# Performance work log

Hardware: AMD Instinct MI355X
Metric: run time of the kernel (lower is better)

The kernel has to match this reference:

```python
import jax, jax.numpy as jnp
import numpy as np

EMBED_DIM = 1024
NUM_HEADS = 16
HEAD_DIM = EMBED_DIM // NUM_HEADS
SCALE = HEAD_DIM ** -0.5


def setup_inputs() -> dict:
    key = jax.random.key(0)
    ks = jax.random.split(key, 9)
    B, N = 2, 2048
    s = EMBED_DIM ** -0.5  # ~ torch Linear init scale
    x = jax.random.normal(ks[0], (B, N, EMBED_DIM), dtype=jnp.float32)
    Wq = jax.random.uniform(ks[1], (EMBED_DIM, EMBED_DIM), jnp.float32, -s, s)
    bq = jax.random.uniform(ks[2], (EMBED_DIM,), jnp.float32, -s, s)
    Wk = jax.random.uniform(ks[3], (EMBED_DIM, EMBED_DIM), jnp.float32, -s, s)
    bk = jax.random.uniform(ks[4], (EMBED_DIM,), jnp.float32, -s, s)
    Wv = jax.random.uniform(ks[5], (EMBED_DIM, EMBED_DIM), jnp.float32, -s, s)
    bv = jax.random.uniform(ks[6], (EMBED_DIM,), jnp.float32, -s, s)
    Wo = jax.random.uniform(ks[7], (EMBED_DIM, EMBED_DIM), jnp.float32, -s, s)
    bo = jax.random.uniform(ks[8], (EMBED_DIM,), jnp.float32, -s, s)
    return {"x": x, "Wq": Wq, "bq": bq, "Wk": Wk, "bk": bk,
            "Wv": Wv, "bv": bv, "Wo": Wo, "bo": bo}


def reference(x, Wq, bq, Wk, bk, Wv, bv, Wo, bo):
    B, N, R = x.shape
    H, D = NUM_HEADS, HEAD_DIM
    # projections: Linear(x) = x @ W^T + b; reshape to (B, H, N, D)
    def proj(W, b):
        return (x @ W.T + b).reshape(B, N, H, D).transpose(0, 2, 1, 3)
    q = proj(Wq, bq)
    k = proj(Wk, bk)
    v = proj(Wv, bv)
    attn = jnp.einsum('bhnd,bhmd->bhnm', q, k) * SCALE  # (B,H,N,N)
    attn = jax.nn.softmax(attn, axis=-1)
    out = jnp.einsum('bhnm,bhmd->bhnd', attn, v)        # (B,H,N,D)
    out = out.transpose(0, 2, 1, 3).reshape(B, N, R)
    return out @ Wo.T + bo
```

## Files before the change

### kernel.cpp

```cpp
#include <hip/hip_runtime.h>
#include <stdint.h>

typedef __bf16 bf16;
typedef __bf16 bf16x4 __attribute__((ext_vector_type(4)));
typedef __bf16 bf16x8 __attribute__((ext_vector_type(8)));
typedef float f32x4 __attribute__((ext_vector_type(4)));

#define MFMA16(a, b, c) __builtin_amdgcn_mfma_f32_16x16x32_bf16((a), (b), (c), 0, 0, 0)

#define EMBED 1024
#define SEQ   2048
#define MROWS 4096
#define ATTN_QSCALE 0.1803368801111f

__device__ __forceinline__ void gl2lds16(const bf16* g, bf16* l) {
    __builtin_amdgcn_global_load_lds(
        (const __attribute__((address_space(1))) void*)g,
        (__attribute__((address_space(3))) void*)l,
        16, 0, 0);
}

__global__ __launch_bounds__(256) void cast_all_kernel(
    const float* __restrict__ x,  const float* __restrict__ Wq,
    const float* __restrict__ Wk, const float* __restrict__ Wv,
    const float* __restrict__ Wo, bf16* __restrict__ dst) {
    const int blk = blockIdx.x;
    const float* src;
    size_t so, dofs;
    if (blk < 2048) {
        src = x; so = (size_t)blk * 2048; dofs = so;
    } else {
        const int w = (blk - 2048) >> 9;
        so  = (size_t)((blk - 2048) & 511) * 2048;
        src = (w == 0) ? Wq : (w == 1) ? Wk : (w == 2) ? Wv : Wo;
        dofs = (size_t)(4 + w) * 1024 * 1024 + so;
    }
    const size_t i = (size_t)threadIdx.x * 8;
    float4 a = *(const float4*)(src + so + i);
    float4 b = *(const float4*)(src + so + i + 4);
    bf16x8 o;
    o[0] = (bf16)a.x; o[1] = (bf16)a.y; o[2] = (bf16)a.z; o[3] = (bf16)a.w;
    o[4] = (bf16)b.x; o[5] = (bf16)b.y; o[6] = (bf16)b.z; o[7] = (bf16)b.w;
    *(bf16x8*)(dst + dofs + i) = o;
}

template <bool SCALE>
__device__ __forceinline__ void gemm_tile(const bf16* __restrict__ A,
                                          const bf16* __restrict__ W,
                                          const float* __restrict__ bias,
                                          bf16* __restrict__ C,
                                          int m0, int n0, bf16* smem) {
    const int lane = threadIdx.x & 63;
    const int wv   = threadIdx.x >> 6;
    const int wm   = (wv >> 1) * 64;
    const int wn   = (wv & 1) * 64;
    const int fr   = lane & 15;
    const int quad = lane >> 4;
    const int srow = wv * 16 + (lane >> 2);
    const int swz  = ((lane & 3) ^ ((lane >> 2) & 3) ^ ((lane >> 4) & 3)) * 8;
    const int fcol = (quad ^ (fr & 3) ^ (fr >> 2)) * 8;

    f32x4 acc[4][4];
#pragma unroll
    for (int mt = 0; mt < 4; ++mt)
#pragma unroll
        for (int nt = 0; nt < 4; ++nt)
            acc[mt][nt] = (f32x4){0.f, 0.f, 0.f, 0.f};

    auto stage = [&](int kt, int bb) {
        bf16* As = smem + bb * 8192;
        bf16* Bs = As + 4096;
        const int k0 = kt * 32;
#pragma unroll
        for (int c = 0; c < 2; ++c) {
            gl2lds16(A + (size_t)(m0 + c * 64 + srow) * 1024 + k0 + swz,
                     &As[(c * 64 + wv * 16) * 32]);
            gl2lds16(W + (size_t)(n0 + c * 64 + srow) * 1024 + k0 + swz,
                     &Bs[(c * 64 + wv * 16) * 32]);
        }
    };

    stage(0, 0);
    stage(1, 1);
#pragma unroll
    for (int kt = 0; kt < 32; ++kt) {
        if (kt < 31) asm volatile("s_waitcnt vmcnt(4)" ::: "memory");
        else         asm volatile("s_waitcnt vmcnt(0)" ::: "memory");
        __builtin_amdgcn_s_barrier();
        if (kt < 30) stage(kt + 2, (kt + 2) % 3);
        const bf16* As = smem + (kt % 3) * 8192;
        const bf16* Bs = As + 4096;
        bf16x8 af[4], bfr[4];
#pragma unroll
        for (int t = 0; t < 4; ++t) {
            af[t]  = *(const bf16x8*)&As[(wm + t * 16 + fr) * 32 + fcol];
            bfr[t] = *(const bf16x8*)&Bs[(wn + t * 16 + fr) * 32 + fcol];
        }
        __builtin_amdgcn_s_setprio(1);
#pragma unroll
        for (int mt = 0; mt < 4; ++mt)
#pragma unroll
            for (int nt = 0; nt < 4; ++nt)
                acc[mt][nt] = MFMA16(af[mt], bfr[nt], acc[mt][nt]);
        __builtin_amdgcn_s_setprio(0);
    }

    float bv[4];
#pragma unroll
    for (int nt = 0; nt < 4; ++nt)
        bv[nt] = bias[n0 + wn + nt * 16 + fr];
    const int row4 = quad * 4;
#pragma unroll
    for (int mt = 0; mt < 4; ++mt)
#pragma unroll
        for (int nt = 0; nt < 4; ++nt)
#pragma unroll
            for (int r = 0; r < 4; ++r) {
                int m = m0 + wm + mt * 16 + row4 + r;
                int n = n0 + wn + nt * 16 + fr;
                float v = acc[mt][nt][r] + bv[nt];
                if (SCALE) v *= ATTN_QSCALE;
                C[(size_t)m * 1024 + n] = (bf16)v;
            }
}

__device__ __forceinline__ void v_tile(const bf16* __restrict__ x,
                                       const bf16* __restrict__ Wv,
                                       const float* __restrict__ bias,
                                       bf16* __restrict__ VT,
                                       int m0, int n0, bf16* smem) {
    const int lane = threadIdx.x & 63;
    const int wv   = threadIdx.x >> 6;
    const int wmW  = (wv >> 1) * 64;
    const int wnT  = (wv & 1) * 64;
    const int f    = lane & 15;
    const int quad = lane >> 4;
    const int srow = wv * 16 + (lane >> 2);
    const int swz  = ((lane & 3) ^ ((lane >> 2) & 3) ^ ((lane >> 4) & 3)) * 8;
    const int fcol = (quad ^ (f & 3) ^ (f >> 2)) * 8;

    f32x4 acc[4][4];
#pragma unroll
    for (int mt = 0; mt < 4; ++mt)
#pragma unroll
        for (int nt = 0; nt < 4; ++nt)
            acc[mt][nt] = (f32x4){0.f, 0.f, 0.f, 0.f};

    auto stage = [&](int kt, int bb) {
        bf16* As = smem + bb * 8192;
        bf16* Bs = As + 4096;
        const int k0 = kt * 32;
#pragma unroll
        for (int c = 0; c < 2; ++c) {
            gl2lds16(x  + (size_t)(m0 + c * 64 + srow) * 1024 + k0 + swz,
                     &As[(c * 64 + wv * 16) * 32]);
            gl2lds16(Wv + (size_t)(n0 + c * 64 + srow) * 1024 + k0 + swz,
                     &Bs[(c * 64 + wv * 16) * 32]);
        }
    };

    stage(0, 0);
    stage(1, 1);
#pragma unroll
    for (int kt = 0; kt < 32; ++kt) {
        if (kt < 31) asm volatile("s_waitcnt vmcnt(4)" ::: "memory");
        else         asm volatile("s_waitcnt vmcnt(0)" ::: "memory");
        __builtin_amdgcn_s_barrier();
        if (kt < 30) stage(kt + 2, (kt + 2) % 3);
        const bf16* As = smem + (kt % 3) * 8192;
        const bf16* Bs = As + 4096;
        bf16x8 wf[4], xf[4];
#pragma unroll
        for (int t = 0; t < 4; ++t) {
            wf[t] = *(const bf16x8*)&Bs[(wmW + t * 16 + f) * 32 + fcol];
            xf[t] = *(const bf16x8*)&As[(wnT + t * 16 + f) * 32 + fcol];
        }
        __builtin_amdgcn_s_setprio(1);
#pragma unroll
        for (int mt = 0; mt < 4; ++mt)
#pragma unroll
            for (int nt = 0; nt < 4; ++nt)
                acc[mt][nt] = MFMA16(wf[mt], xf[nt], acc[mt][nt]);
        __builtin_amdgcn_s_setprio(0);
    }

    float4 b4[4];
#pragma unroll
    for (int mt = 0; mt < 4; ++mt)
        b4[mt] = *(const float4*)&bias[n0 + wmW + mt * 16 + quad * 4];

    __syncthreads();

#pragma unroll
    for (int mt = 0; mt < 4; ++mt)
#pragma unroll
        for (int nt = 0; nt < 4; ++nt) {
            const int tok = wnT + nt * 16 + f;
#pragma unroll
            for (int r = 0; r < 4; ++r) {
                const float bvr = (r == 0) ? b4[mt].x : (r == 1) ? b4[mt].y
                                : (r == 2) ? b4[mt].z : b4[mt].w;
                smem[(wmW + mt * 16 + quad * 4 + r) * 136 + tok] =
                    (bf16)(acc[mt][nt][r] + bvr);
            }
        }
    __syncthreads();

    const int n_r  = threadIdx.x >> 4;
    const int t8   = (threadIdx.x & 15) * 8;
    const int base = t8 & ~31;
    const int u4   = ((t8 >> 3) & 3) * 4;
    const int bb   = m0 >> 11;
    const int tokg = (m0 & 2047) + t8;
#pragma unroll
    for (int p = 0; p < 8; ++p) {
        const int n_loc = p * 16 + n_r;
        const bf16* row = &smem[n_loc * 136];
        bf16x4 a = *(const bf16x4*)&row[base + u4];
        bf16x4 b = *(const bf16x4*)&row[base + 16 + u4];
        bf16x8 v = {a[0], a[1], a[2], a[3], b[0], b[1], b[2], b[3]};
        *(bf16x8*)&VT[((size_t)(bb * 1024 + n0 + n_loc)) * 2048 + tokg] = v;
    }
}

__global__ __launch_bounds__(256) void qkv_kernel(
    const bf16* __restrict__ x,
    const bf16* __restrict__ Wq, const float* __restrict__ bq,
    const bf16* __restrict__ Wk, const float* __restrict__ bk,
    const bf16* __restrict__ Wv, const float* __restrict__ bv,
    bf16* __restrict__ Q, bf16* __restrict__ K, bf16* __restrict__ VT) {
    __shared__ __align__(16) bf16 smem[24576];
    const int m0    = blockIdx.x * 128;
    const int which = blockIdx.y >> 3;
    const int n0    = (blockIdx.y & 7) * 128;
    if (which == 0)      gemm_tile<true>(x, Wq, bq, Q, m0, n0, smem);
    else if (which == 1) gemm_tile<false>(x, Wk, bk, K, m0, n0, smem);
    else                 v_tile(x, Wv, bv, VT, m0, n0, smem);
}

__global__ __launch_bounds__(256) void oproj_kernel(
    const bf16* __restrict__ A, const bf16* __restrict__ W,
    const float* __restrict__ bias, float* __restrict__ C) {
    const int m0 = blockIdx.x * 128;
    const int n0 = blockIdx.y * 64;

    __shared__ __align__(16) bf16 smem[18432];

    const int lane = threadIdx.x & 63;
    const int wv   = threadIdx.x >> 6;
    const int wm   = (wv >> 1) * 64;
    const int wn   = (wv & 1) * 32;
    const int fr   = lane & 15;
    const int quad = lane >> 4;
    const int srow = wv * 16 + (lane >> 2);
    const int swz  = ((lane & 3) ^ ((lane >> 2) & 3) ^ ((lane >> 4) & 3)) * 8;
    const int fcol = (quad ^ (fr & 3) ^ (fr >> 2)) * 8;

    f32x4 acc[4][2];
#pragma unroll
    for (int mt = 0; mt < 4; ++mt)
#pragma unroll
        for (int nt = 0; nt < 2; ++nt)
            acc[mt][nt] = (f32x4){0.f, 0.f, 0.f, 0.f};

    auto stage = [&](int kt, int bb) {
        bf16* As = smem + bb * 6144;
        bf16* Bs = As + 4096;
        const int k0 = kt * 32;
#pragma unroll
        for (int c = 0; c < 2; ++c)
            gl2lds16(A + (size_t)(m0 + c * 64 + srow) * 1024 + k0 + swz,
                     &As[(c * 64 + wv * 16) * 32]);
        gl2lds16(W + (size_t)(n0 + srow) * 1024 + k0 + swz,
                 &Bs[(wv * 16) * 32]);
    };

    stage(0, 0);
    stage(1, 1);
#pragma unroll
    for (int kt = 0; kt < 32; ++kt) {
        if (kt < 31) asm volatile("s_waitcnt vmcnt(3)" ::: "memory");
        else         asm volatile("s_waitcnt vmcnt(0)" ::: "memory");
        __builtin_amdgcn_s_barrier();
        if (kt < 30) stage(kt + 2, (kt + 2) % 3);
        const bf16* As = smem + (kt % 3) * 6144;
        const bf16* Bs = As + 4096;
        bf16x8 af[4], bfr[2];
#pragma unroll
        for (int t = 0; t < 4; ++t)
            af[t] = *(const bf16x8*)&As[(wm + t * 16 + fr) * 32 + fcol];
#pragma unroll
        for (int t = 0; t < 2; ++t)
            bfr[t] = *(const bf16x8*)&Bs[(wn + t * 16 + fr) * 32 + fcol];
        __builtin_amdgcn_s_setprio(1);
#pragma unroll
        for (int mt = 0; mt < 4; ++mt)
#pragma unroll
            for (int nt = 0; nt < 2; ++nt)
                acc[mt][nt] = MFMA16(af[mt], bfr[nt], acc[mt][nt]);
        __builtin_amdgcn_s_setprio(0);
    }

    float bv[2];
#pragma unroll
    for (int nt = 0; nt < 2; ++nt)
        bv[nt] = bias[n0 + wn + nt * 16 + fr];
    const int row4 = quad * 4;
#pragma unroll
    for (int mt = 0; mt < 4; ++mt)
#pragma unroll
        for (int nt = 0; nt < 2; ++nt)
#pragma unroll
            for (int r = 0; r < 4; ++r) {
                int m = m0 + wm + mt * 16 + row4 + r;
                int n = n0 + wn + nt * 16 + fr;
                C[(size_t)m * 1024 + n] = acc[mt][nt][r] + bv[nt];
            }
}

__global__ __launch_bounds__(256, 2) void attn_kernel(
    const bf16* __restrict__ Q, const bf16* __restrict__ K,
    const bf16* __restrict__ VT, bf16* __restrict__ O) {
    const int tid  = threadIdx.x;
    const int lane = tid & 63;
    const int wv   = tid >> 6;
    const int quad = lane >> 4;
    const int f    = lane & 15;
    const int lin  = blockIdx.y * 16 + blockIdx.x;
    const int sw   = (lin & 7) * 64 + (lin >> 3);
    const int qt   = sw & 15;
    const int bh   = sw >> 4;
    const int q0   = qt * 128;
    const int b    = bh >> 4;
    const int h    = bh & 15;

    const bf16* Qp = Q + ((size_t)b * SEQ) * 1024 + (size_t)h * 64;
    const bf16* Kp = K + ((size_t)b * SEQ) * 1024 + (size_t)h * 64;
    const bf16* Vp = VT + ((size_t)(b * 1024 + h * 64)) * 2048;
    bf16* Op = O + ((size_t)b * SEQ) * 1024 + (size_t)h * 64;

    __shared__ bf16 Ks[4][64 * 64];
    __shared__ bf16 VTs[4][64 * 64];

    bf16x8 qf[2][2];
#pragma unroll
    for (int qg = 0; qg < 2; ++qg) {
        const bf16* qrow = Qp + (size_t)(q0 + wv * 32 + qg * 16 + f) * 1024;
        qf[qg][0] = *(const bf16x8*)(qrow + quad * 8);
        qf[qg][1] = *(const bf16x8*)(qrow + 32 + quad * 8);
    }

    const int srow = wv * 8 + (lane >> 3);
    const int swz  = (((lane & 7) ^ ((lane >> 3) & 7))) * 8;
    auto stageK = [&](int t, int bb) {
        const int kv0 = t * 64;
#pragma unroll
        for (int i = 0; i < 2; ++i)
            gl2lds16(Kp + (size_t)(kv0 + i * 32 + srow) * 1024 + swz,
                     &Ks[bb][(i * 32 + wv * 8) * 64]);
    };
    auto stageVT = [&](int t, int bb) {
        const int kv0 = t * 64;
#pragma unroll
        for (int i = 0; i < 2; ++i)
            gl2lds16(Vp + (size_t)(i * 32 + srow) * 2048 + kv0 + swz,
                     &VTs[bb][(i * 32 + wv * 8) * 64]);
    };

    stageK(0, 0); stageVT(0, 0);
    stageK(1, 1); stageVT(1, 1);

    f32x4 oacc[2][4];
#pragma unroll
    for (int qg = 0; qg < 2; ++qg)
#pragma unroll
        for (int t = 0; t < 4; ++t)
            oacc[qg][t] = (f32x4){0.f, 0.f, 0.f, 0.f};
    f32x4 lacc[2];
#pragma unroll
    for (int qg = 0; qg < 2; ++qg)
        lacc[qg] = (f32x4){0.f, 0.f, 0.f, 0.f};
    const bf16x8 ones8 = {(bf16)1.f, (bf16)1.f, (bf16)1.f, (bf16)1.f,
                          (bf16)1.f, (bf16)1.f, (bf16)1.f, (bf16)1.f};
    const f32x4  zero4 = (f32x4){0.f, 0.f, 0.f, 0.f};

    const int fcol0 = (quad ^ (f & 7)) * 8;
    const int fcol1 = ((4 + quad) ^ (f & 7)) * 8;

    bf16x8 pbA[2][2], pbB[2][2];

    asm volatile("s_waitcnt vmcnt(4)" ::: "memory");
    __builtin_amdgcn_s_barrier();
    {
        bf16x8 kf0[4], kf1[4];
#pragma unroll
        for (int t4 = 0; t4 < 4; ++t4) {
            kf0[t4] = *(const bf16x8*)&Ks[0][(t4 * 16 + f) * 64 + fcol0];
            kf1[t4] = *(const bf16x8*)&Ks[0][(t4 * 16 + f) * 64 + fcol1];
        }
#pragma unroll
        for (int qg = 0; qg < 2; ++qg) {
            f32x4 s[4];
            __builtin_amdgcn_s_setprio(1);
#pragma unroll
            for (int t4 = 0; t4 < 4; ++t4) {
                s[t4] = MFMA16(kf0[t4], qf[qg][0], zero4);
                s[t4] = MFMA16(kf1[t4], qf[qg][1], s[t4]);
            }
            __builtin_amdgcn_s_setprio(0);
#pragma unroll
            for (int kt = 0; kt < 2; ++kt) {
#pragma unroll
                for (int r = 0; r < 4; ++r) {
                    pbA[qg][kt][r]     = (bf16)__builtin_amdgcn_exp2f(s[2 * kt][r]);
                    pbA[qg][kt][4 + r] = (bf16)__builtin_amdgcn_exp2f(s[2 * kt + 1][r]);
                }
                lacc[qg] = MFMA16(ones8, pbA[qg][kt], lacc[qg]);
            }
        }
    }

    auto step = [&](int t, bf16x8 (&pbc)[2][2], bf16x8 (&pbn)[2][2],
                    int drain, bool doStage, bool doQK) {
        if (doStage) { stageK(t + 2, (t + 2) & 3); stageVT(t + 2, (t + 2) & 3); }
        if (drain == 4) asm volatile("s_waitcnt vmcnt(4)" ::: "memory");
        else            asm volatile("s_waitcnt vmcnt(0)" ::: "memory");
        __builtin_amdgcn_s_barrier();
        const int bq = (t + 1) & 3;
        const int bp = t & 3;

        bf16x8 kf0[4], kf1[4];
        if (doQK) {
#pragma unroll
            for (int t4 = 0; t4 < 4; ++t4) {
                kf0[t4] = *(const bf16x8*)&Ks[bq][(t4 * 16 + f) * 64 + fcol0];
                kf1[t4] = *(const bf16x8*)&Ks[bq][(t4 * 16 + f) * 64 + fcol1];
            }
        }
#pragma unroll
        for (int u = 0; u < 4; ++u) {
            f32x4 s[4];
            const bool qk = doQK && u < 2;
            if (qk) {
                __builtin_amdgcn_s_setprio(1);
#pragma unroll
                for (int t4 = 0; t4 < 4; ++t4) {
                    s[t4] = MFMA16(kf0[t4], qf[u][0], zero4);
                    s[t4] = MFMA16(kf1[t4], qf[u][1], s[t4]);
                }
                __builtin_amdgcn_s_setprio(0);
            }
            __builtin_amdgcn_s_setprio(1);
#pragma unroll
            for (int kt = 0; kt < 2; ++kt) {
                const int pc = ((kt * 4 + quad) ^ (f & 7)) * 8;
                bf16x8 vf = *(const bf16x8*)&VTs[bp][(u * 16 + f) * 64 + pc];
#pragma unroll
                for (int qg = 0; qg < 2; ++qg)
                    oacc[qg][u] = MFMA16(vf, pbc[qg][kt], oacc[qg][u]);
            }
            __builtin_amdgcn_s_setprio(0);
            if (qk) {
#pragma unroll
                for (int kt = 0; kt < 2; ++kt) {
#pragma unroll
                    for (int r = 0; r < 4; ++r) {
                        pbn[u][kt][r]     = (bf16)__builtin_amdgcn_exp2f(s[2 * kt][r]);
                        pbn[u][kt][4 + r] = (bf16)__builtin_amdgcn_exp2f(s[2 * kt + 1][r]);
                    }
                    lacc[u] = MFMA16(ones8, pbn[u][kt], lacc[u]);
                }
            }
        }
    };

    for (int tt = 0; tt < 30; tt += 2) {
        step(tt,     pbA, pbB, 4, true, true);
        step(tt + 1, pbB, pbA, 4, true, true);
    }
    step(30, pbA, pbB, 0, false, true);
    step(31, pbB, pbA, 0, false, false);

#pragma unroll
    for (int qg = 0; qg < 2; ++qg) {
        const float inv = 1.0f / lacc[qg][0];
        const int q = q0 + wv * 32 + qg * 16 + f;
        bf16* orow = Op + (size_t)q * 1024;
#pragma unroll
        for (int dt = 0; dt < 4; ++dt) {
            bf16x4 ov;
#pragma unroll
            for (int r = 0; r < 4; ++r)
                ov[r] = (bf16)(oacc[qg][dt][r] * inv);
            *(bf16x4*)(orow + dt * 16 + quad * 4) = ov;
        }
    }
}

extern "C" void kernel_launch(void* const* d_in, const int* in_sizes, int n_in,
                              void* d_out, int out_size, void* d_ws, size_t ws_size,
                              hipStream_t stream) {
    const float* x  = (const float*)d_in[0];
    const float* Wq = (const float*)d_in[1];
    const float* bq = (const float*)d_in[2];
    const float* Wk = (const float*)d_in[3];
    const float* bk = (const float*)d_in[4];
    const float* Wv = (const float*)d_in[5];
    const float* bv = (const float*)d_in[6];
    const float* Wo = (const float*)d_in[7];
    const float* bo = (const float*)d_in[8];
    float* out = (float*)d_out;

    bf16* xb    = (bf16*)d_ws;
    bf16* Wqb   = xb   + (size_t)MROWS * 1024;
    bf16* Wkb   = Wqb  + (size_t)1024 * 1024;
    bf16* Wvb   = Wkb  + (size_t)1024 * 1024;
    bf16* Wob   = Wvb  + (size_t)1024 * 1024;
    bf16* Q     = Wob  + (size_t)1024 * 1024;
    bf16* K     = Q    + (size_t)MROWS * 1024;
    bf16* VT    = K    + (size_t)MROWS * 1024;
    bf16* O     = VT   + (size_t)MROWS * 1024;

    cast_all_kernel<<<4096, 256, 0, stream>>>(x, Wq, Wk, Wv, Wo, xb);

    qkv_kernel<<<dim3(32, 24), 256, 0, stream>>>(xb, Wqb, bq, Wkb, bk, Wvb, bv, Q, K, VT);
    attn_kernel<<<dim3(16, 32), 256, 0, stream>>>(Q, K, VT, O);
    oproj_kernel<<<dim3(32, 16), 256, 0, stream>>>(O, Wob, bo, out);
}
```

Baseline: 175.1 us.

## Halve attention query tile to 64 rows and triple-buffer K/V for occupancy

The attention kernel now gives each block 64 query rows instead of 128, so each wave owns one 16-row query group. The grid doubles to 1024 blocks, LDS buffering drops from four stages to three, and launch bounds ask for three blocks per CU. K fragments are now loaded from LDS inside the QK loop rather than preloaded, and the wait uses vmcnt(0) before the barrier with staging issued after it. This trades K/V reuse per block, since each K/V tile is now loaded twice as often, for lower register and LDS use and more parallelism to hide latency.

```diff
diff --git a/kernel.cpp b/kernel.cpp
--- a/kernel.cpp
+++ b/kernel.cpp
@@ -318,7 +318,7 @@
             }
 }
 
-__global__ __launch_bounds__(256, 2) void attn_kernel(
+__global__ __launch_bounds__(256, 3) void attn_kernel(
     const bf16* __restrict__ Q, const bf16* __restrict__ K,
     const bf16* __restrict__ VT, bf16* __restrict__ O) {
     const int tid  = threadIdx.x;
@@ -326,11 +326,11 @@
     const int wv   = tid >> 6;
     const int quad = lane >> 4;
     const int f    = lane & 15;
-    const int lin  = blockIdx.y * 16 + blockIdx.x;
-    const int sw   = (lin & 7) * 64 + (lin >> 3);
-    const int qt   = sw & 15;
-    const int bh   = sw >> 4;
-    const int q0   = qt * 128;
+    const int lin  = blockIdx.y * 32 + blockIdx.x;
+    const int sw   = (lin & 7) * 128 + (lin >> 3);
+    const int qt   = sw & 31;
+    const int bh   = sw >> 5;
+    const int q0   = qt * 64;
     const int b    = bh >> 4;
     const int h    = bh & 15;
 
@@ -339,15 +339,14 @@
     const bf16* Vp = VT + ((size_t)(b * 1024 + h * 64)) * 2048;
     bf16* Op = O + ((size_t)b * SEQ) * 1024 + (size_t)h * 64;
 
-    __shared__ bf16 Ks[4][64 * 64];
-    __shared__ bf16 VTs[4][64 * 64];
-
-    bf16x8 qf[2][2];
-#pragma unroll
-    for (int qg = 0; qg < 2; ++qg) {
-        const bf16* qrow = Qp + (size_t)(q0 + wv * 32 + qg * 16 + f) * 1024;
-        qf[qg][0] = *(const bf16x8*)(qrow + quad * 8);
-        qf[qg][1] = *(const bf16x8*)(qrow + 32 + quad * 8);
+    __shared__ bf16 Ks[3][64 * 64];
+    __shared__ bf16 VTs[3][64 * 64];
+
+    bf16x8 qf0, qf1;
+    {
+        const bf16* qrow = Qp + (size_t)(q0 + wv * 16 + f) * 1024;
+        qf0 = *(const bf16x8*)(qrow + quad * 8);
+        qf1 = *(const bf16x8*)(qrow + 32 + quad * 8);
     }
 
     const int srow = wv * 8 + (lane >> 3);
@@ -370,16 +369,11 @@
     stageK(0, 0); stageVT(0, 0);
     stageK(1, 1); stageVT(1, 1);
 
-    f32x4 oacc[2][4];
-#pragma unroll
-    for (int qg = 0; qg < 2; ++qg)
-#pragma unroll
-        for (int t = 0; t < 4; ++t)
-            oacc[qg][t] = (f32x4){0.f, 0.f, 0.f, 0.f};
-    f32x4 lacc[2];
-#pragma unroll
-    for (int qg = 0; qg < 2; ++qg)
-        lacc[qg] = (f32x4){0.f, 0.f, 0.f, 0.f};
+    f32x4 oacc[4];
+#pragma unroll
+    for (int t = 0; t < 4; ++t)
+        oacc[t] = (f32x4){0.f, 0.f, 0.f, 0.f};
+    f32x4 lacc = (f32x4){0.f, 0.f, 0.f, 0.f};
     const bf16x8 ones8 = {(bf16)1.f, (bf16)1.f, (bf16)1.f, (bf16)1.f,
                           (bf16)1.f, (bf16)1.f, (bf16)1.f, (bf16)1.f};
     const f32x4  zero4 = (f32x4){0.f, 0.f, 0.f, 0.f};
@@ -387,66 +381,51 @@
     const int fcol0 = (quad ^ (f & 7)) * 8;
     const int fcol1 = ((4 + quad) ^ (f & 7)) * 8;
 
-    bf16x8 pbA[2][2], pbB[2][2];
+    bf16x8 pbA[2], pbB[2];
 
     asm volatile("s_waitcnt vmcnt(4)" ::: "memory");
     __builtin_amdgcn_s_barrier();
     {
-        bf16x8 kf0[4], kf1[4];
+        f32x4 s[4];
+        __builtin_amdgcn_s_setprio(1);
 #pragma unroll
         for (int t4 = 0; t4 < 4; ++t4) {
-            kf0[t4] = *(const bf16x8*)&Ks[0][(t4 * 16 + f) * 64 + fcol0];
-            kf1[t4] = *(const bf16x8*)&Ks[0][(t4 * 16 + f) * 64 + fcol1];
-        }
-#pragma unroll
-        for (int qg = 0; qg < 2; ++qg) {
-            f32x4 s[4];
-            __builtin_amdgcn_s_setprio(1);
-#pragma unroll
-            for (int t4 = 0; t4 < 4; ++t4) {
-                s[t4] = MFMA16(kf0[t4], qf[qg][0], zero4);
-                s[t4] = MFMA16(kf1[t4], qf[qg][1], s[t4]);
-            }
-            __builtin_amdgcn_s_setprio(0);
-#pragma unroll
-            for (int kt = 0; kt < 2; ++kt) {
-#pragma unroll
-                for (int r = 0; r < 4; ++r) {
-                    pbA[qg][kt][r]     = (bf16)__builtin_amdgcn_exp2f(s[2 * kt][r]);
-                    pbA[qg][kt][4 + r] = (bf16)__builtin_amdgcn_exp2f(s[2 * kt + 1][r]);
-                }
-                lacc[qg] = MFMA16(ones8, pbA[qg][kt], lacc[qg]);
-            }
-        }
-    }
-
-    auto step = [&](int t, bf16x8 (&pbc)[2][2], bf16x8 (&pbn)[2][2],
-                    int drain, bool doStage, bool doQK) {
-        if (doStage) { stageK(t + 2, (t + 2) & 3); stageVT(t + 2, (t + 2) & 3); }
-        if (drain == 4) asm volatile("s_waitcnt vmcnt(4)" ::: "memory");
-        else            asm volatile("s_waitcnt vmcnt(0)" ::: "memory");
+            bf16x8 k0 = *(const bf16x8*)&Ks[0][(t4 * 16 + f) * 64 + fcol0];
+            bf16x8 k1 = *(const bf16x8*)&Ks[0][(t4 * 16 + f) * 64 + fcol1];
+            s[t4] = MFMA16(k0, qf0, zero4);
+            s[t4] = MFMA16(k1, qf1, s[t4]);
+        }
+        __builtin_amdgcn_s_setprio(0);
+#pragma unroll
+        for (int kt = 0; kt < 2; ++kt) {
+#pragma unroll
+            for (int r = 0; r < 4; ++r) {
+                pbA[kt][r]     = (bf16)__builtin_amdgcn_exp2f(s[2 * kt][r]);
+                pbA[kt][4 + r] = (bf16)__builtin_amdgcn_exp2f(s[2 * kt + 1][r]);
+            }
+            lacc = MFMA16(ones8, pbA[kt], lacc);
+        }
+    }
+
+    auto step = [&](int t, bf16x8 (&pbc)[2], bf16x8 (&pbn)[2], bool doQK) {
+        asm volatile("s_waitcnt vmcnt(0)" ::: "memory");
         __builtin_amdgcn_s_barrier();
-        const int bq = (t + 1) & 3;
-        const int bp = t & 3;
-
-        bf16x8 kf0[4], kf1[4];
-        if (doQK) {
-#pragma unroll
-            for (int t4 = 0; t4 < 4; ++t4) {
-                kf0[t4] = *(const bf16x8*)&Ks[bq][(t4 * 16 + f) * 64 + fcol0];
-                kf1[t4] = *(const bf16x8*)&Ks[bq][(t4 * 16 + f) * 64 + fcol1];
-            }
-        }
+        if (t < 30) { stageK(t + 2, (t + 2) % 3); stageVT(t + 2, (t + 2) % 3); }
+        const int bq = (t + 1) % 3;
+        const int bp = t % 3;
+
+        f32x4 s[4];
 #pragma unroll
         for (int u = 0; u < 4; ++u) {
-            f32x4 s[4];
-            const bool qk = doQK && u < 2;
-            if (qk) {
+            if (doQK && u < 2) {
                 __builtin_amdgcn_s_setprio(1);
 #pragma unroll
-                for (int t4 = 0; t4 < 4; ++t4) {
-                    s[t4] = MFMA16(kf0[t4], qf[u][0], zero4);
-                    s[t4] = MFMA16(kf1[t4], qf[u][1], s[t4]);
+                for (int j = 0; j < 2; ++j) {
+                    const int t4 = u * 2 + j;
+                    bf16x8 k0 = *(const bf16x8*)&Ks[bq][(t4 * 16 + f) * 64 + fcol0];
+                    bf16x8 k1 = *(const bf16x8*)&Ks[bq][(t4 * 16 + f) * 64 + fcol1];
+                    s[t4] = MFMA16(k0, qf0, zero4);
+                    s[t4] = MFMA16(k1, qf1, s[t4]);
                 }
                 __builtin_amdgcn_s_setprio(0);
             }
@@ -455,43 +434,38 @@
             for (int kt = 0; kt < 2; ++kt) {
                 const int pc = ((kt * 4 + quad) ^ (f & 7)) * 8;
                 bf16x8 vf = *(const bf16x8*)&VTs[bp][(u * 16 + f) * 64 + pc];
-#pragma unroll
-                for (int qg = 0; qg < 2; ++qg)
-                    oacc[qg][u] = MFMA16(vf, pbc[qg][kt], oacc[qg][u]);
+                oacc[u] = MFMA16(vf, pbc[kt], oacc[u]);
             }
             __builtin_amdgcn_s_setprio(0);
-            if (qk) {
-#pragma unroll
-                for (int kt = 0; kt < 2; ++kt) {
-#pragma unroll
-                    for (int r = 0; r < 4; ++r) {
-                        pbn[u][kt][r]     = (bf16)__builtin_amdgcn_exp2f(s[2 * kt][r]);
-                        pbn[u][kt][4 + r] = (bf16)__builtin_amdgcn_exp2f(s[2 * kt + 1][r]);
-                    }
-                    lacc[u] = MFMA16(ones8, pbn[u][kt], lacc[u]);
+            if (doQK && u >= 2) {
+                const int kt = u - 2;
+#pragma unroll
+                for (int r = 0; r < 4; ++r) {
+                    pbn[kt][r]     = (bf16)__builtin_amdgcn_exp2f(s[2 * kt][r]);
+                    pbn[kt][4 + r] = (bf16)__builtin_amdgcn_exp2f(s[2 * kt + 1][r]);
                 }
+                lacc = MFMA16(ones8, pbn[kt], lacc);
             }
         }
     };
 
     for (int tt = 0; tt < 30; tt += 2) {
-        step(tt,     pbA, pbB, 4, true, true);
-        step(tt + 1, pbB, pbA, 4, true, true);
-    }
-    step(30, pbA, pbB, 0, false, true);
-    step(31, pbB, pbA, 0, false, false);
-
-#pragma unroll
-    for (int qg = 0; qg < 2; ++qg) {
-        const float inv = 1.0f / lacc[qg][0];
-        const int q = q0 + wv * 32 + qg * 16 + f;
+        step(tt,     pbA, pbB, true);
+        step(tt + 1, pbB, pbA, true);
+    }
+    step(30, pbA, pbB, true);
+    step(31, pbB, pbA, false);
+
+    {
+        const float inv = 1.0f / lacc[0];
+        const int q = q0 + wv * 16 + f;
         bf16* orow = Op + (size_t)q * 1024;
 #pragma unroll
         for (int dt = 0; dt < 4; ++dt) {
             bf16x4 ov;
 #pragma unroll
             for (int r = 0; r < 4; ++r)
-                ov[r] = (bf16)(oacc[qg][dt][r] * inv);
+                ov[r] = (bf16)(oacc[dt][r] * inv);
             *(bf16x4*)(orow + dt * 16 + quad * 4) = ov;
         }
     }
@@ -524,6 +498,6 @@
     cast_all_kernel<<<4096, 256, 0, stream>>>(x, Wq, Wk, Wv, Wo, xb);
 
     qkv_kernel<<<dim3(32, 24), 256, 0, stream>>>(xb, Wqb, bq, Wkb, bk, Wvb, bv, Q, K, VT);
-    attn_kernel<<<dim3(16, 32), 256, 0, stream>>>(Q, K, VT, O);
+    attn_kernel<<<dim3(32, 32), 256, 0, stream>>>(Q, K, VT, O);
     oproj_kernel<<<dim3(32, 16), 256, 0, stream>>>(O, Wob, bo, out);
 }
```

Result: slower. 195.3 us (+11.6%).

## Use 256x128 tiles for Q/K projections and flatten QKV grid

Applied to the files above, without the earlier changes.

The Q and K projection tiles grow from 128x128 to 256x128, so each wave computes 8x4 MFMA tiles and A-fragments are loaded one at a time inside the M loop. Each staged W tile is now reused across more rows, and the Q/K block count halves, so the QKV grid becomes 512 blocks in a 1D layout (128 Q, 128 K, 256 V). Shared memory grows to 72 KB for the three-buffer pipeline, and launch bounds request 2 blocks per CU. The risks are higher register pressure from 128 accumulator floats, fewer blocks, and unequal work between the Q/K blocks and the V blocks.

```diff
diff --git a/kernel.cpp b/kernel.cpp
--- a/kernel.cpp
+++ b/kernel.cpp
@@ -45,14 +45,14 @@
 }
 
 template <bool SCALE>
-__device__ __forceinline__ void gemm_tile(const bf16* __restrict__ A,
-                                          const bf16* __restrict__ W,
-                                          const float* __restrict__ bias,
-                                          bf16* __restrict__ C,
-                                          int m0, int n0, bf16* smem) {
+__device__ __forceinline__ void gemm_tile256(const bf16* __restrict__ A,
+                                             const bf16* __restrict__ W,
+                                             const float* __restrict__ bias,
+                                             bf16* __restrict__ C,
+                                             int m0, int n0, bf16* smem) {
     const int lane = threadIdx.x & 63;
     const int wv   = threadIdx.x >> 6;
-    const int wm   = (wv >> 1) * 64;
+    const int wm   = (wv >> 1) * 128;
     const int wn   = (wv & 1) * 64;
     const int fr   = lane & 15;
     const int quad = lane >> 4;
@@ -60,48 +60,49 @@
     const int swz  = ((lane & 3) ^ ((lane >> 2) & 3) ^ ((lane >> 4) & 3)) * 8;
     const int fcol = (quad ^ (fr & 3) ^ (fr >> 2)) * 8;
 
-    f32x4 acc[4][4];
-#pragma unroll
-    for (int mt = 0; mt < 4; ++mt)
+    f32x4 acc[8][4];
+#pragma unroll
+    for (int mt = 0; mt < 8; ++mt)
 #pragma unroll
         for (int nt = 0; nt < 4; ++nt)
             acc[mt][nt] = (f32x4){0.f, 0.f, 0.f, 0.f};
 
     auto stage = [&](int kt, int bb) {
-        bf16* As = smem + bb * 8192;
-        bf16* Bs = As + 4096;
+        bf16* As = smem + bb * 12288;
+        bf16* Bs = As + 8192;
         const int k0 = kt * 32;
 #pragma unroll
-        for (int c = 0; c < 2; ++c) {
+        for (int c = 0; c < 4; ++c)
             gl2lds16(A + (size_t)(m0 + c * 64 + srow) * 1024 + k0 + swz,
                      &As[(c * 64 + wv * 16) * 32]);
+#pragma unroll
+        for (int c = 0; c < 2; ++c)
             gl2lds16(W + (size_t)(n0 + c * 64 + srow) * 1024 + k0 + swz,
                      &Bs[(c * 64 + wv * 16) * 32]);
-        }
     };
 
     stage(0, 0);
     stage(1, 1);
 #pragma unroll
     for (int kt = 0; kt < 32; ++kt) {
-        if (kt < 31) asm volatile("s_waitcnt vmcnt(4)" ::: "memory");
+        if (kt < 31) asm volatile("s_waitcnt vmcnt(6)" ::: "memory");
         else         asm volatile("s_waitcnt vmcnt(0)" ::: "memory");
         __builtin_amdgcn_s_barrier();
         if (kt < 30) stage(kt + 2, (kt + 2) % 3);
-        const bf16* As = smem + (kt % 3) * 8192;
-        const bf16* Bs = As + 4096;
-        bf16x8 af[4], bfr[4];
-#pragma unroll
-        for (int t = 0; t < 4; ++t) {
-            af[t]  = *(const bf16x8*)&As[(wm + t * 16 + fr) * 32 + fcol];
+        const bf16* As = smem + (kt % 3) * 12288;
+        const bf16* Bs = As + 8192;
+        bf16x8 bfr[4];
+#pragma unroll
+        for (int t = 0; t < 4; ++t)
             bfr[t] = *(const bf16x8*)&Bs[(wn + t * 16 + fr) * 32 + fcol];
-        }
         __builtin_amdgcn_s_setprio(1);
 #pragma unroll
-        for (int mt = 0; mt < 4; ++mt)
+        for (int mt = 0; mt < 8; ++mt) {
+            bf16x8 af = *(const bf16x8*)&As[(wm + mt * 16 + fr) * 32 + fcol];
 #pragma unroll
             for (int nt = 0; nt < 4; ++nt)
-                acc[mt][nt] = MFMA16(af[mt], bfr[nt], acc[mt][nt]);
+                acc[mt][nt] = MFMA16(af, bfr[nt], acc[mt][nt]);
+        }
         __builtin_amdgcn_s_setprio(0);
     }
 
@@ -111,7 +112,7 @@
         bv[nt] = bias[n0 + wn + nt * 16 + fr];
     const int row4 = quad * 4;
 #pragma unroll
-    for (int mt = 0; mt < 4; ++mt)
+    for (int mt = 0; mt < 8; ++mt)
 #pragma unroll
         for (int nt = 0; nt < 4; ++nt)
 #pragma unroll
@@ -223,19 +224,23 @@
     }
 }
 
-__global__ __launch_bounds__(256) void qkv_kernel(
+__global__ __launch_bounds__(256, 2) void qkv_kernel(
     const bf16* __restrict__ x,
     const bf16* __restrict__ Wq, const float* __restrict__ bq,
     const bf16* __restrict__ Wk, const float* __restrict__ bk,
     const bf16* __restrict__ Wv, const float* __restrict__ bv,
     bf16* __restrict__ Q, bf16* __restrict__ K, bf16* __restrict__ VT) {
-    __shared__ __align__(16) bf16 smem[24576];
-    const int m0    = blockIdx.x * 128;
-    const int which = blockIdx.y >> 3;
-    const int n0    = (blockIdx.y & 7) * 128;
-    if (which == 0)      gemm_tile<true>(x, Wq, bq, Q, m0, n0, smem);
-    else if (which == 1) gemm_tile<false>(x, Wk, bk, K, m0, n0, smem);
-    else                 v_tile(x, Wv, bv, VT, m0, n0, smem);
+    __shared__ __align__(16) bf16 smem[36864];
+    const int id = blockIdx.x;
+    if (id < 128) {
+        gemm_tile256<true>(x, Wq, bq, Q, (id >> 3) * 256, (id & 7) * 128, smem);
+    } else if (id < 256) {
+        const int t = id - 128;
+        gemm_tile256<false>(x, Wk, bk, K, (t >> 3) * 256, (t & 7) * 128, smem);
+    } else {
+        const int t = id - 256;
+        v_tile(x, Wv, bv, VT, (t >> 3) * 128, (t & 7) * 128, smem);
+    }
 }
 
 __global__ __launch_bounds__(256) void oproj_kernel(
@@ -523,7 +528,7 @@
 
     cast_all_kernel<<<4096, 256, 0, stream>>>(x, Wq, Wk, Wv, Wo, xb);
 
-    qkv_kernel<<<dim3(32, 24), 256, 0, stream>>>(xb, Wqb, bq, Wkb, bk, Wvb, bv, Q, K, VT);
+    qkv_kernel<<<512, 256, 0, stream>>>(xb, Wqb, bq, Wkb, bk, Wvb, bv, Q, K, VT);
     attn_kernel<<<dim3(16, 32), 256, 0, stream>>>(Q, K, VT, O);
     oproj_kernel<<<dim3(32, 16), 256, 0, stream>>>(O, Wob, bo, out);
 }
```

New measurement: 174.3 us (median of 2 runs). No clear change (-0.4%).
